# Optimization experiments

Hardware: AMD Instinct MI355X
Metric: run time of the kernel (lower is better)

The kernel has to match this reference:

```python
import jax, jax.numpy as jnp
import numpy as np

B, T, I, H, O = 4096, 512, 1, 50, 1


def setup_inputs() -> dict:
    key = jax.random.key(0)
    ks = jax.random.split(key, 7)
    s = 1.0 / np.sqrt(H)  # torch LSTM/Linear default init scale
    x = jax.random.normal(ks[0], (B, T, I), dtype=jnp.float32)
    W_ih = jax.random.uniform(ks[1], (4 * H, I), jnp.float32, -s, s)
    W_hh = jax.random.uniform(ks[2], (4 * H, H), jnp.float32, -s, s)
    b_ih = jax.random.uniform(ks[3], (4 * H,), jnp.float32, -s, s)
    b_hh = jax.random.uniform(ks[4], (4 * H,), jnp.float32, -s, s)
    W_fc = jax.random.uniform(ks[5], (O, H), jnp.float32, -s, s)
    b_fc = jax.random.uniform(ks[6], (O,), jnp.float32, -s, s)
    return {"x": x, "W_ih": W_ih, "W_hh": W_hh, "b_ih": b_ih,
            "b_hh": b_hh, "W_fc": W_fc, "b_fc": b_fc}


def reference(x, W_ih, W_hh, b_ih, b_hh, W_fc, b_fc):
    # x: [B, T, I]. Precompute input projections for all timesteps: [B, T, 4H]
    xp = jnp.einsum('bti,gi->btg', x, W_ih) + (b_ih + b_hh)

    def step(carry, xt):
        h, c = carry  # [B, H] each
        gates = xt + h @ W_hh.T  # [B, 4H]; torch gate order: i, f, g, o
        i, f, g, o = jnp.split(gates, 4, axis=-1)
        c = jax.nn.sigmoid(f) * c + jax.nn.sigmoid(i) * jnp.tanh(g)
        h = jax.nn.sigmoid(o) * jnp.tanh(c)
        return (h, c), None

    h0 = jnp.zeros((x.shape[0], W_hh.shape[1]), x.dtype)
    (h_last, _), _ = jax.lax.scan(step, (h0, h0), jnp.swapaxes(xp, 0, 1))
    # final-timestep hidden -> Linear
    return h_last @ W_fc.T + b_fc  # [B, O]
```

## Files before the change

kernel.cpp:

```cpp
#include <hip/hip_runtime.h>
#include <math.h>

#define T_LEN 512
#define H_DIM 50
#define BPB   16
#define NW    12
#define L2E   1.44269504088896f
#define XSTR  520

typedef _Float16 half8_t __attribute__((ext_vector_type(8)));
typedef float    f32x4_t __attribute__((ext_vector_type(4)));

__device__ __forceinline__ f32x4_t mfma16(half8_t a, half8_t b, f32x4_t c) {
#if defined(__HIP_DEVICE_COMPILE__)
    return __builtin_amdgcn_mfma_f32_16x16x32_f16(a, b, c, 0, 0, 0);
#else
    return c;
#endif
}
__device__ __forceinline__ int pk16(float a, float b) {
    return __builtin_bit_cast(int, __builtin_amdgcn_cvt_pkrtz(a, b));
}

__global__ __launch_bounds__(NW * 64, 1) void lstm_mfma(
    const float* __restrict__ x,
    const float* __restrict__ W_ih,
    const float* __restrict__ W_hh,
    const float* __restrict__ b_ih,
    const float* __restrict__ b_hh,
    const float* __restrict__ W_fc,
    const float* __restrict__ b_fc,
    float* __restrict__ out)
{
    const int tid = threadIdx.x;
    const int w   = tid >> 6;
    const int L   = tid & 63;
    const int col = L & 15;
    const int g4  = L >> 4;

    __shared__ _Float16 xls[BPB][XSTR];
    __shared__ __align__(16) _Float16 hb[2][8][BPB][8];

    {
        const float4* xg4 = reinterpret_cast<const float4*>(
            x + (size_t)blockIdx.x * BPB * T_LEN);
        for (int f = tid; f < BPB * T_LEN / 4; f += NW * 64) {
            const float4 v = xg4[f];
            const int bb = f >> 7;
            const int c0 = (f & 127) << 2;
            *reinterpret_cast<int*>(&xls[bb][c0])     = pk16(v.x, v.y);
            *reinterpret_cast<int*>(&xls[bb][c0 + 2]) = pk16(v.z, v.w);
        }
    }
    for (int i = tid; i < 1024; i += NW * 64) reinterpret_cast<int*>(hb)[i] = 0;
    __syncthreads();
    if (tid < BPB) hb[0][6][tid][2] = xls[tid][0];

    auto load_pair = [&](int p, half8_t& f0, half8_t& f1) {
        const int uA = p >> 2, gA = p & 3;
        const float sA = (gA == 2) ? (-2.0f * L2E) : (-L2E);
        #pragma unroll
        for (int j = 0; j < 8; ++j) {
            const int k0 = 8 * g4 + j;
            const int k1 = 32 + k0;
            float v0 = 0.0f, v1 = 0.0f;
            if (uA < H_DIM) {
                const int r = gA * H_DIM + uA;
                v0 = W_hh[r * H_DIM + k0];
                if (k1 < H_DIM)       v1 = W_hh[r * H_DIM + k1];
                else if (k1 == H_DIM) v1 = W_ih[r];
            }
            f0[j] = (_Float16)(v0 * sA);
            f1[j] = (_Float16)(v1 * sA);
        }
    };
    half8_t a0, a1, a20, a21;
    load_pair(16 * w + col, a0, a1);
    load_pair(192 + col, a20, a21);

    auto load_bias = [&](int uD) -> f32x4_t {
        f32x4_t bc;
        #pragma unroll
        for (int j = 0; j < 4; ++j) {
            const float sj = (j == 2) ? (-2.0f * L2E) : (-L2E);
            bc[j] = (uD < H_DIM)
                  ? (b_ih[j * H_DIM + uD] + b_hh[j * H_DIM + uD]) * sj : 0.0f;
        }
        return bc;
    };
    const int uD1 = 4 * w + g4;
    const int uD2 = 48 + g4;
    const f32x4_t biasC1 = load_bias(uD1);
    const f32x4_t biasC2 = load_bias(uD2);

    const int uD2w = (uD2 < H_DIM) ? uD2 : (52 + (uD2 & 1));
    _Float16* hw1 = &hb[0][uD1 >> 3][col][uD1 & 7];
    _Float16* hw2 = &hb[0][uD2w >> 3][col][uD2w & 7];
    const _Float16* rB = &hb[0][0][0][0] + (g4 * 128 + col * 8);
    const _Float16* xq = &xls[col][1];
    _Float16* xd = &hb[0][6][col][2];
    const bool xw  = (w == 9) && (g4 == 3);
    const bool two = (w == 11);

    float c1 = 0.0f, c2 = 0.0f;
    __syncthreads();

    auto update = [&](const f32x4_t& acc, float& c, _Float16* hw, int WO) {
        const float Ei = __builtin_amdgcn_exp2f(acc[0]);
        const float Ef = __builtin_amdgcn_exp2f(acc[1]);
        const float Eg = __builtin_amdgcn_exp2f(acc[2]);
        const float Eo = __builtin_amdgcn_exp2f(acc[3]);
        const float fg  = __builtin_amdgcn_rcpf(1.0f + Ef);
        const float r1  = __builtin_amdgcn_rcpf((1.0f + Ei) * (1.0f + Eg));
        const float pig = (1.0f - Eg) * r1;
        c = __fmaf_rn(fg, c, pig);
        const float Ec = __builtin_amdgcn_exp2f(c * (-2.0f * L2E));
        const float r2 = __builtin_amdgcn_rcpf((1.0f + Ec) * (1.0f + Eo));
        const float hv = (1.0f - Ec) * r2;
        hw[WO] = (_Float16)hv;
    };

    auto step = [&](int RO, int WO, int XI) {
        const half8_t b0 = *reinterpret_cast<const half8_t*>(rB + RO);
        const half8_t b1 = *reinterpret_cast<const half8_t*>(rB + RO + 512);
        _Float16 xn = (_Float16)0.0f;
        if (xw) xn = xq[XI];
        f32x4_t acc = mfma16(a0, b0, biasC1);
        acc = mfma16(a1, b1, acc);
        update(acc, c1, hw1, WO);
        if (two) {
            f32x4_t acc2 = mfma16(a20, b0, biasC2);
            acc2 = mfma16(a21, b1, acc2);
            update(acc2, c2, hw2, WO);
        }
        if (xw) xd[WO] = xn;
        __syncthreads();
    };

    for (int t = 0; t < T_LEN; t += 4) {
        step(0,    1024, 0);
        step(1024, 0,    1);
        step(0,    1024, 2);
        step(1024, 0,    3);
        xq += 4;
    }

    if (w == 0) {
        float part = 0.0f;
        #pragma unroll
        for (int j = 0; j < 13; ++j) {
            const int u = 13 * g4 + j;
            if (u < H_DIM)
                part += (float)hb[0][u >> 3][col][u & 7] * W_fc[u];
        }
        part += __shfl_xor(part, 16);
        part += __shfl_xor(part, 32);
        if (L < BPB) out[blockIdx.x * BPB + L] = part + b_fc[0];
    }
}

extern "C" void kernel_launch(void* const* d_in, const int* in_sizes, int n_in,
                              void* d_out, int out_size, void* d_ws, size_t ws_size,
                              hipStream_t stream) {
    const float* x    = (const float*)d_in[0];
    const float* W_ih = (const float*)d_in[1];
    const float* W_hh = (const float*)d_in[2];
    const float* b_ih = (const float*)d_in[3];
    const float* b_hh = (const float*)d_in[4];
    const float* W_fc = (const float*)d_in[5];
    const float* b_fc = (const float*)d_in[6];
    float* out = (float*)d_out;

    const int B = in_sizes[0] / T_LEN;
    lstm_mfma<<<dim3(B / BPB), dim3(NW * 64), 0, stream>>>(
        x, W_ih, W_hh, b_ih, b_hh, W_fc, b_fc, out);
}
```

Baseline: 194.2 us.

## Consolidate LSTM step onto four waves with three gate tiles each

Cuts the block from 12 waves to 4. Each wave now issues three MFMA tiles per timestep, and wave 3 also handles the leftover tile. This lowers the cost of the per-step __syncthreads barrier and raises the independent MFMA work inside each wave, which helps hide latency. The trade-off is more serial transcendental and update work per wave on the critical path of each timestep, plus higher register use.

Measured after the change: 217.1 us. 1.12x slower.

```diff
diff --git a/kernel.cpp b/kernel.cpp
--- a/kernel.cpp
+++ b/kernel.cpp
@@ -4,7 +4,8 @@
 #define T_LEN 512
 #define H_DIM 50
 #define BPB   16
-#define NW    12
+#define NW    4
+#define TPW   3
 #define L2E   1.44269504088896f
 #define XSTR  520
 
@@ -74,10 +75,6 @@
             f1[j] = (_Float16)(v1 * sA);
         }
     };
-    half8_t a0, a1, a20, a21;
-    load_pair(16 * w + col, a0, a1);
-    load_pair(192 + col, a20, a21);
-
     auto load_bias = [&](int uD) -> f32x4_t {
         f32x4_t bc;
         #pragma unroll
@@ -88,24 +85,36 @@
         }
         return bc;
     };
-    const int uD1 = 4 * w + g4;
-    const int uD2 = 48 + g4;
-    const f32x4_t biasC1 = load_bias(uD1);
-    const f32x4_t biasC2 = load_bias(uD2);
 
-    const int uD2w = (uD2 < H_DIM) ? uD2 : (52 + (uD2 & 1));
-    _Float16* hw1 = &hb[0][uD1 >> 3][col][uD1 & 7];
-    _Float16* hw2 = &hb[0][uD2w >> 3][col][uD2w & 7];
+    half8_t A0[TPW], A1[TPW];
+    f32x4_t BC[TPW];
+    _Float16* hw[TPW];
+    #pragma unroll
+    for (int i = 0; i < TPW; ++i) {
+        const int m = TPW * w + i;
+        load_pair(16 * m + col, A0[i], A1[i]);
+        const int uD = 4 * m + g4;
+        BC[i] = load_bias(uD);
+        hw[i] = &hb[0][uD >> 3][col][uD & 7];
+    }
+    half8_t T0, T1;
+    f32x4_t BC3 = {0.f, 0.f, 0.f, 0.f};
+    _Float16* hw3 = &hb[0][6][col][g4 & 1];
+    if (w == 3) {
+        load_pair(192 + col, T0, T1);
+        BC3 = load_bias(48 + g4);
+    }
+
     const _Float16* rB = &hb[0][0][0][0] + (g4 * 128 + col * 8);
     const _Float16* xq = &xls[col][1];
     _Float16* xd = &hb[0][6][col][2];
-    const bool xw  = (w == 9) && (g4 == 3);
-    const bool two = (w == 11);
+    const bool xw = (w == 0) && (g4 == 3);
 
-    float c1 = 0.0f, c2 = 0.0f;
+    float c[TPW] = {0.f, 0.f, 0.f};
+    float c3 = 0.0f;
     __syncthreads();
 
-    auto update = [&](const f32x4_t& acc, float& c, _Float16* hw, int WO) {
+    auto update = [&](const f32x4_t& acc, float& cc, _Float16* hwp, int WO) {
         const float Ei = __builtin_amdgcn_exp2f(acc[0]);
         const float Ef = __builtin_amdgcn_exp2f(acc[1]);
         const float Eg = __builtin_amdgcn_exp2f(acc[2]);
@@ -113,11 +122,11 @@
         const float fg  = __builtin_amdgcn_rcpf(1.0f + Ef);
         const float r1  = __builtin_amdgcn_rcpf((1.0f + Ei) * (1.0f + Eg));
         const float pig = (1.0f - Eg) * r1;
-        c = __fmaf_rn(fg, c, pig);
-        const float Ec = __builtin_amdgcn_exp2f(c * (-2.0f * L2E));
+        cc = __fmaf_rn(fg, cc, pig);
+        const float Ec = __builtin_amdgcn_exp2f(cc * (-2.0f * L2E));
         const float r2 = __builtin_amdgcn_rcpf((1.0f + Ec) * (1.0f + Eo));
         const float hv = (1.0f - Ec) * r2;
-        hw[WO] = (_Float16)hv;
+        hwp[WO] = (_Float16)hv;
     };
 
     auto step = [&](int RO, int WO, int XI) {
@@ -125,14 +134,18 @@
         const half8_t b1 = *reinterpret_cast<const half8_t*>(rB + RO + 512);
         _Float16 xn = (_Float16)0.0f;
         if (xw) xn = xq[XI];
-        f32x4_t acc = mfma16(a0, b0, biasC1);
-        acc = mfma16(a1, b1, acc);
-        update(acc, c1, hw1, WO);
-        if (two) {
-            f32x4_t acc2 = mfma16(a20, b0, biasC2);
-            acc2 = mfma16(a21, b1, acc2);
-            update(acc2, c2, hw2, WO);
+        f32x4_t acc[TPW];
+        #pragma unroll
+        for (int i = 0; i < TPW; ++i) acc[i] = mfma16(A0[i], b0, BC[i]);
+        #pragma unroll
+        for (int i = 0; i < TPW; ++i) acc[i] = mfma16(A1[i], b1, acc[i]);
+        if (w == 3) {
+            f32x4_t a3 = mfma16(T0, b0, BC3);
+            a3 = mfma16(T1, b1, a3);
+            if (L < 32) update(a3, c3, hw3, WO);
         }
+        #pragma unroll
+        for (int i = 0; i < TPW; ++i) update(acc[i], c[i], hw[i], WO);
         if (xw) xd[WO] = xn;
         __syncthreads();
     };
```
